# Performance work log

Hardware: AMD Instinct MI355X
Metric: run time of the kernel (lower is better)

Reference implementation:

```python
import jax, jax.numpy as jnp
import numpy as np

DIM = 128
B = 262144


def setup_inputs() -> dict:
    key = jax.random.key(0)
    k_t, k_w1, k_b1, k_w2, k_b2 = jax.random.split(key, 5)
    t = jax.random.uniform(k_t, (B,), dtype=jnp.float32)  # t in [0, 1]
    s = 1.0 / np.sqrt(DIM)  # torch Linear default init scale
    W1 = jax.random.uniform(k_w1, (DIM, DIM), dtype=jnp.float32, minval=-s, maxval=s)
    b1 = jax.random.uniform(k_b1, (DIM,), dtype=jnp.float32, minval=-s, maxval=s)
    W2 = jax.random.uniform(k_w2, (DIM, DIM), dtype=jnp.float32, minval=-s, maxval=s)
    b2 = jax.random.uniform(k_b2, (DIM,), dtype=jnp.float32, minval=-s, maxval=s)
    return {"t": t, "W1": W1, "b1": b1, "W2": W2, "b2": b2}


def reference(t, W1, b1, W2, b2):
    # create_timestep_embedding, vectorized over batch and dim:
    #   emb[b, i] = t[b]*cos(i/dim*pi*t[b]) + t[b]*sin(i/dim*pi*(1 - t[b]))
    phase = (jnp.arange(DIM, dtype=t.dtype) / DIM) * jnp.pi  # [DIM]
    tb = t[:, None]  # [B, 1]
    emb = tb * jnp.cos(phase[None, :] * tb) + tb * jnp.sin(phase[None, :] * (1.0 - tb))  # [B, DIM]
    x = jax.nn.silu(emb @ W1.T + b1)  # Linear128 + SiLU
    x = jax.nn.silu(x @ W2.T + b2)    # Linear128 + SiLU
    return x
```

## Files before the change

kernel.cpp:

```cpp
#include <hip/hip_runtime.h>

typedef _Float16 f16;
typedef _Float16 f16x2 __attribute__((ext_vector_type(2)));
typedef _Float16 f16x8 __attribute__((ext_vector_type(8)));
typedef float    f32x4 __attribute__((ext_vector_type(4)));

#define DIM 128

__device__ __forceinline__ float silu_f(float x) {
    float e = __builtin_amdgcn_exp2f(x * -1.44269504088896341f);
    return x * __builtin_amdgcn_rcpf(1.0f + e);
}

__global__ __launch_bounds__(256, 3)
void ts_mlp_kernel(const float* __restrict__ t,
                   const float* __restrict__ W1, const float* __restrict__ b1,
                   const float* __restrict__ W2, const float* __restrict__ b2,
                   float* __restrict__ out, int B) {
    __shared__ f16x8 embf[4][4][64];
    __shared__ f16x2 x1s[1024][4];

    const int tid  = threadIdx.x;
    const int wv   = tid >> 6;
    const int lane = tid & 63;
    const int q    = lane >> 4;
    const int ln   = lane & 15;
    const int par  = lane & 1;

    const int ntiles = B >> 6;

    float t4[4];
#pragma unroll
    for (int ti = 0; ti < 4; ++ti) {
        const int tile = blockIdx.x * 4 + ti;
        t4[ti] = (tile < ntiles) ? t[tile * 64 + wv * 16 + ln] : 0.0f;
    }

    f16x8 w1f[4][2], w2f[4][2];
    float b1v[2], b2v[2];
#pragma unroll
    for (int u = 0; u < 2; ++u) {
        const int n = wv * 32 + u * 16 + ln;
        b1v[u] = b1[n];
        b2v[u] = b2[n];
#pragma unroll
        for (int kt = 0; kt < 4; ++kt) {
            const float4* p1 = (const float4*)(W1 + n * DIM + kt * 32 + q * 8);
            const float4* p2 = (const float4*)(W2 + n * DIM + kt * 32 + q * 8);
            const float4 a = p1[0], b = p1[1], c = p2[0], d = p2[1];
            f16x8 f1, f2;
            f1[0]=(f16)a.x; f1[1]=(f16)a.y; f1[2]=(f16)a.z; f1[3]=(f16)a.w;
            f1[4]=(f16)b.x; f1[5]=(f16)b.y; f1[6]=(f16)b.z; f1[7]=(f16)b.w;
            f2[0]=(f16)c.x; f2[1]=(f16)c.y; f2[2]=(f16)c.z; f2[3]=(f16)c.w;
            f2[4]=(f16)d.x; f2[5]=(f16)d.y; f2[6]=(f16)d.z; f2[7]=(f16)d.w;
            w1f[kt][u] = f1;
            w2f[kt][u] = f2;
        }
    }

#pragma unroll 1
    for (int ti = 0; ti < 4; ++ti) {
        const int tile = blockIdx.x * 4 + ti;
        if (tile >= ntiles) break;
        const int row0 = tile * 64;

        const float tv   = t4[ti];
        const float t256 = tv * 0.00390625f;
        const float o256 = (1.0f - tv) * 0.00390625f;
        const float qb   = (float)(q * 8);
#pragma unroll
        for (int kt = 0; kt < 4; ++kt) {
            f16x8 ef;
#pragma unroll
            for (int j = 0; j < 8; ++j) {
                const float fd = (float)(kt * 32 + j) + qb;
                const float c  = __builtin_amdgcn_cosf(fd * t256);
                const float s  = __builtin_amdgcn_sinf(fd * o256);
                ef[j] = (f16)(tv * (c + s));
            }
            embf[wv][kt][lane] = ef;
        }
        __syncthreads();

        f32x4 acc[4][2];
#pragma unroll
        for (int mt = 0; mt < 4; ++mt) {
            acc[mt][0] = (f32x4){0.f,0.f,0.f,0.f};
            acc[mt][1] = (f32x4){0.f,0.f,0.f,0.f};
#pragma unroll
            for (int kt = 0; kt < 4; ++kt) {
                const f16x8 af = embf[mt][kt][lane];
                acc[mt][0] = __builtin_amdgcn_mfma_f32_16x16x32_f16(af, w1f[kt][0], acc[mt][0], 0, 0, 0);
                acc[mt][1] = __builtin_amdgcn_mfma_f32_16x16x32_f16(af, w1f[kt][1], acc[mt][1], 0, 0, 0);
            }
        }

#pragma unroll
        for (int mt = 0; mt < 4; ++mt) {
#pragma unroll
            for (int u = 0; u < 2; ++u) {
                float v[4], pv[4];
#pragma unroll
                for (int r = 0; r < 4; ++r) v[r] = silu_f(acc[mt][u][r] + b1v[u]);
#pragma unroll
                for (int r = 0; r < 4; ++r) pv[r] = __shfl_xor(v[r], 1, 64);
                const int k0  = wv * 32 + u * 16 + (ln & 14);
                const int cch = k0 >> 3;
                const int hw  = (k0 & 7) >> 1;
#pragma unroll
                for (int p = 0; p < 2; ++p) {
                    const int r = par * 2 + p;
                    const int m = mt * 16 + q * 4 + r;
                    const float lo = par ? pv[r] : v[r];
                    const float hi = par ? v[r] : pv[r];
                    f16x2 h; h.x = (f16)lo; h.y = (f16)hi;
                    x1s[m * 16 + (cch ^ (m & 15))][hw] = h;
                }
            }
        }
        __syncthreads();

#pragma unroll
        for (int mt = 0; mt < 4; ++mt) {
            f32x4 a2c[2];
            a2c[0] = (f32x4){0.f,0.f,0.f,0.f};
            a2c[1] = (f32x4){0.f,0.f,0.f,0.f};
#pragma unroll
            for (int kt = 0; kt < 4; ++kt) {
                const int m = mt * 16 + ln;
                const f16x8 a2 = *(const f16x8*)&x1s[m * 16 + ((kt * 4 + q) ^ ln)][0];
                a2c[0] = __builtin_amdgcn_mfma_f32_16x16x32_f16(a2, w2f[kt][0], a2c[0], 0, 0, 0);
                a2c[1] = __builtin_amdgcn_mfma_f32_16x16x32_f16(a2, w2f[kt][1], a2c[1], 0, 0, 0);
            }
#pragma unroll
            for (int u = 0; u < 2; ++u) {
                const int col = wv * 32 + u * 16 + ln;
                const size_t rbase = (size_t)(row0 + mt * 16 + q * 4) * DIM + col;
#pragma unroll
                for (int r = 0; r < 4; ++r) {
                    out[rbase + (size_t)r * DIM] = silu_f(a2c[u][r] + b2v[u]);
                }
            }
        }
        __syncthreads();
    }
}

extern "C" void kernel_launch(void* const* d_in, const int* in_sizes, int n_in,
                              void* d_out, int out_size, void* d_ws, size_t ws_size,
                              hipStream_t stream) {
    const float* t  = (const float*)d_in[0];
    const float* W1 = (const float*)d_in[1];
    const float* b1 = (const float*)d_in[2];
    const float* W2 = (const float*)d_in[3];
    const float* b2 = (const float*)d_in[4];
    float* out = (float*)d_out;
    const int B = in_sizes[0];
    const int ntiles = B >> 6;
    const int grid = (ntiles + 3) >> 2;
    ts_mlp_kernel<<<dim3(grid), dim3(256), 0, stream>>>(t, W1, b1, W2, b2, out, B);
}
```

Measured before the change: 221.6 us.

## Stage output through LDS for coalesced float4 stores, one tile per block

Each block now handles a single 64-row tile instead of looping over four, so the grid grows fourfold and weights are reloaded per tile. The second-layer results go into a swizzled shared-memory staging buffer that reuses the embedding/activation space through a union. They are then written to global memory as fully coalesced float4 rows instead of scattered per-lane scalar stores. Launch bounds are raised to four blocks per CU. The trade-offs are more weight-load and conversion traffic per output row, extra barriers, and the 32KB staging buffer, which may limit occupancy.

```diff
diff --git a/kernel.cpp b/kernel.cpp
--- a/kernel.cpp
+++ b/kernel.cpp
@@ -12,13 +12,15 @@
     return x * __builtin_amdgcn_rcpf(1.0f + e);
 }
 
-__global__ __launch_bounds__(256, 3)
+__global__ __launch_bounds__(256, 4)
 void ts_mlp_kernel(const float* __restrict__ t,
                    const float* __restrict__ W1, const float* __restrict__ b1,
                    const float* __restrict__ W2, const float* __restrict__ b2,
                    float* __restrict__ out, int B) {
-    __shared__ f16x8 embf[4][4][64];
-    __shared__ f16x2 x1s[1024][4];
+    __shared__ union SH {
+        struct { f16x8 embf[4][4][64]; f16x2 x1s[1024][4]; } p;
+        float ostage[64 * 128];
+    } sh;
 
     const int tid  = threadIdx.x;
     const int wv   = tid >> 6;
@@ -27,14 +29,9 @@
     const int ln   = lane & 15;
     const int par  = lane & 1;
 
-    const int ntiles = B >> 6;
+    const int row0 = blockIdx.x * 64;
 
-    float t4[4];
-#pragma unroll
-    for (int ti = 0; ti < 4; ++ti) {
-        const int tile = blockIdx.x * 4 + ti;
-        t4[ti] = (tile < ntiles) ? t[tile * 64 + wv * 16 + ln] : 0.0f;
-    }
+    const float tv = t[row0 + wv * 16 + ln];
 
     f16x8 w1f[4][2], w2f[4][2];
     float b1v[2], b2v[2];
@@ -58,13 +55,7 @@
         }
     }
 
-#pragma unroll 1
-    for (int ti = 0; ti < 4; ++ti) {
-        const int tile = blockIdx.x * 4 + ti;
-        if (tile >= ntiles) break;
-        const int row0 = tile * 64;
-
-        const float tv   = t4[ti];
+    {
         const float t256 = tv * 0.00390625f;
         const float o256 = (1.0f - tv) * 0.00390625f;
         const float qb   = (float)(q * 8);
@@ -78,71 +69,89 @@
                 const float s  = __builtin_amdgcn_sinf(fd * o256);
                 ef[j] = (f16)(tv * (c + s));
             }
-            embf[wv][kt][lane] = ef;
+            sh.p.embf[wv][kt][lane] = ef;
         }
-        __syncthreads();
+    }
+    __syncthreads();
 
-        f32x4 acc[4][2];
+    f32x4 acc[4][2];
+#pragma unroll
+    for (int mt = 0; mt < 4; ++mt) {
+        acc[mt][0] = (f32x4){0.f,0.f,0.f,0.f};
+        acc[mt][1] = (f32x4){0.f,0.f,0.f,0.f};
+#pragma unroll
+        for (int kt = 0; kt < 4; ++kt) {
+            const f16x8 af = sh.p.embf[mt][kt][lane];
+            acc[mt][0] = __builtin_amdgcn_mfma_f32_16x16x32_f16(af, w1f[kt][0], acc[mt][0], 0, 0, 0);
+            acc[mt][1] = __builtin_amdgcn_mfma_f32_16x16x32_f16(af, w1f[kt][1], acc[mt][1], 0, 0, 0);
+        }
+    }
+
+#pragma unroll
+    for (int mt = 0; mt < 4; ++mt) {
+#pragma unroll
+        for (int u = 0; u < 2; ++u) {
+            float v[4], pv[4];
+#pragma unroll
+            for (int r = 0; r < 4; ++r) v[r] = silu_f(acc[mt][u][r] + b1v[u]);
+#pragma unroll
+            for (int r = 0; r < 4; ++r) pv[r] = __shfl_xor(v[r], 1, 64);
+            const int k0  = wv * 32 + u * 16 + (ln & 14);
+            const int cch = k0 >> 3;
+            const int hw  = (k0 & 7) >> 1;
+#pragma unroll
+            for (int p = 0; p < 2; ++p) {
+                const int r = par * 2 + p;
+                const int m = mt * 16 + q * 4 + r;
+                const float lo = par ? pv[r] : v[r];
+                const float hi = par ? v[r] : pv[r];
+                f16x2 h; h.x = (f16)lo; h.y = (f16)hi;
+                sh.p.x1s[m * 16 + (cch ^ (m & 15))][hw] = h;
+            }
+        }
+    }
+    __syncthreads();
+
+    f32x4 acc2[4][2];
+#pragma unroll
+    for (int mt = 0; mt < 4; ++mt) {
+        acc2[mt][0] = (f32x4){0.f,0.f,0.f,0.f};
+        acc2[mt][1] = (f32x4){0.f,0.f,0.f,0.f};
+    }
+#pragma unroll
+    for (int kt = 0; kt < 4; ++kt) {
 #pragma unroll
         for (int mt = 0; mt < 4; ++mt) {
-            acc[mt][0] = (f32x4){0.f,0.f,0.f,0.f};
-            acc[mt][1] = (f32x4){0.f,0.f,0.f,0.f};
+            const int m = mt * 16 + ln;
+            const f16x8 a2 = *(const f16x8*)&sh.p.x1s[m * 16 + ((kt * 4 + q) ^ ln)][0];
+            acc2[mt][0] = __builtin_amdgcn_mfma_f32_16x16x32_f16(a2, w2f[kt][0], acc2[mt][0], 0, 0, 0);
+            acc2[mt][1] = __builtin_amdgcn_mfma_f32_16x16x32_f16(a2, w2f[kt][1], acc2[mt][1], 0, 0, 0);
+        }
+    }
+    __syncthreads();
+
 #pragma unroll
-            for (int kt = 0; kt < 4; ++kt) {
-                const f16x8 af = embf[mt][kt][lane];
-                acc[mt][0] = __builtin_amdgcn_mfma_f32_16x16x32_f16(af, w1f[kt][0], acc[mt][0], 0, 0, 0);
-                acc[mt][1] = __builtin_amdgcn_mfma_f32_16x16x32_f16(af, w1f[kt][1], acc[mt][1], 0, 0, 0);
+    for (int mt = 0; mt < 4; ++mt) {
+#pragma unroll
+        for (int u = 0; u < 2; ++u) {
+            const int cc = wv * 8 + u * 4 + (ln >> 2);
+            const int w  = ln & 3;
+#pragma unroll
+            for (int r = 0; r < 4; ++r) {
+                const int m = mt * 16 + q * 4 + r;
+                const float o = silu_f(acc2[mt][u][r] + b2v[u]);
+                sh.ostage[m * 128 + ((cc ^ (m & 7)) << 2) + w] = o;
             }
         }
+    }
+    __syncthreads();
 
 #pragma unroll
-        for (int mt = 0; mt < 4; ++mt) {
-#pragma unroll
-            for (int u = 0; u < 2; ++u) {
-                float v[4], pv[4];
-#pragma unroll
-                for (int r = 0; r < 4; ++r) v[r] = silu_f(acc[mt][u][r] + b1v[u]);
-#pragma unroll
-                for (int r = 0; r < 4; ++r) pv[r] = __shfl_xor(v[r], 1, 64);
-                const int k0  = wv * 32 + u * 16 + (ln & 14);
-                const int cch = k0 >> 3;
-                const int hw  = (k0 & 7) >> 1;
-#pragma unroll
-                for (int p = 0; p < 2; ++p) {
-                    const int r = par * 2 + p;
-                    const int m = mt * 16 + q * 4 + r;
-                    const float lo = par ? pv[r] : v[r];
-                    const float hi = par ? v[r] : pv[r];
-                    f16x2 h; h.x = (f16)lo; h.y = (f16)hi;
-                    x1s[m * 16 + (cch ^ (m & 15))][hw] = h;
-                }
-            }
-        }
-        __syncthreads();
-
-#pragma unroll
-        for (int mt = 0; mt < 4; ++mt) {
-            f32x4 a2c[2];
-            a2c[0] = (f32x4){0.f,0.f,0.f,0.f};
-            a2c[1] = (f32x4){0.f,0.f,0.f,0.f};
-#pragma unroll
-            for (int kt = 0; kt < 4; ++kt) {
-                const int m = mt * 16 + ln;
-                const f16x8 a2 = *(const f16x8*)&x1s[m * 16 + ((kt * 4 + q) ^ ln)][0];
-                a2c[0] = __builtin_amdgcn_mfma_f32_16x16x32_f16(a2, w2f[kt][0], a2c[0], 0, 0, 0);
-                a2c[1] = __builtin_amdgcn_mfma_f32_16x16x32_f16(a2, w2f[kt][1], a2c[1], 0, 0, 0);
-            }
-#pragma unroll
-            for (int u = 0; u < 2; ++u) {
-                const int col = wv * 32 + u * 16 + ln;
-                const size_t rbase = (size_t)(row0 + mt * 16 + q * 4) * DIM + col;
-#pragma unroll
-                for (int r = 0; r < 4; ++r) {
-                    out[rbase + (size_t)r * DIM] = silu_f(a2c[u][r] + b2v[u]);
-                }
-            }
-        }
-        __syncthreads();
+    for (int it = 0; it < 8; ++it) {
+        const int m = it * 8 + (tid >> 5);
+        const int c = tid & 31;
+        const float4 v = *(const float4*)&sh.ostage[m * 128 + ((c ^ (m & 7)) << 2)];
+        *(float4*)(out + (size_t)(row0 + m) * DIM + 4 * c) = v;
     }
 }
 
@@ -156,7 +165,6 @@
     const float* b2 = (const float*)d_in[4];
     float* out = (float*)d_out;
     const int B = in_sizes[0];
-    const int ntiles = B >> 6;
-    const int grid = (ntiles + 3) >> 2;
+    const int grid = B >> 6;
     ts_mlp_kernel<<<dim3(grid), dim3(256), 0, stream>>>(t, W1, b1, W2, b2, out, B);
 }
```

Measured after the change: 225.5 us. No clear change (+1.7%).
